# Performance work log

Measured on AMD Instinct MI355X. Metric: run time of the kernel, lower is better.

Reference implementation:

```python
import jax, jax.numpy as jnp
import numpy as np

HEADS = 24
HEAD_DIM = 96
SPARSE_N = 4
ROPE_BASE = 10000.0


def _rope_cos_sin(pos, D):
    # pos: [L] int positions; D: per-axis rotary dim (even)
    inv_freq = 1.0 / (ROPE_BASE ** (jnp.arange(0, D, 2, dtype=jnp.float32) / D))
    f = pos.astype(jnp.float32)[:, None] * inv_freq[None, :]   # [L, D/2] (interp scale = 1)
    f = jnp.concatenate([f, f], axis=-1)                        # [L, D]
    return jnp.cos(f), jnp.sin(f)


def _rotate_half(x):
    x1, x2 = jnp.split(x, 2, axis=-1)
    return jnp.concatenate([-x2, x1], axis=-1)


def _apply_rope3d(tok, frame, height, width):
    # tok: [b, h, s, d]; RoPE3D splits head_dim into 3 equal chunks for (t, y, x)
    D = tok.shape[-1] // 3
    t = jnp.repeat(jnp.arange(frame), height * width)
    y = jnp.tile(jnp.repeat(jnp.arange(height), width), frame)
    x = jnp.tile(jnp.arange(width), frame * height)
    outs = []
    for i, pos in enumerate((t, y, x)):
        cos, sin = _rope_cos_sin(pos, D)                        # [s, D]
        part = tok[..., i * D:(i + 1) * D]
        outs.append(part * cos[None, None] + _rotate_half(part) * sin[None, None])
    return jnp.concatenate(outs, axis=-1)


def _sparse_1d(x, n):
    # 'b h (g k) d -> (k b) h g d' with pad so s % n*n == 0
    b, h, s, d = x.shape
    pad = (-s) % (n * n)
    if pad:
        x = jnp.pad(x, ((0, 0), (0, 0), (0, pad), (0, 0)))
    g = (s + pad) // n
    x = x.reshape(b, h, g, n, d)
    return jnp.transpose(x, (3, 0, 1, 2, 4)).reshape(n * b, h, g, d), pad


def _reverse_sparse_1d(x, n, s):
    # '(k b) h g d -> b h (g k) d' then crop to s tokens
    kb, h, g, d = x.shape
    b = kb // n
    x = x.reshape(n, b, h, g, d)
    x = jnp.transpose(x, (1, 2, 3, 0, 4)).reshape(b, h, g * n, d)
    return x[:, :, :s, :]


def setup_inputs() -> dict:
    key = jax.random.key(0)
    ks = jax.random.split(key, 5)
    dim = HEADS * HEAD_DIM
    b, f, hh, ww = 1, 8, 16, 32
    s = f * hh * ww
    inp = {
        "hidden_states": jax.random.normal(ks[0], (b, s, dim), dtype=jnp.float32),
        "wq": jax.random.normal(ks[1], (dim, dim), dtype=jnp.float32) * 0.02,
        "bq": jnp.zeros((dim,), jnp.float32),
        "wk": jax.random.normal(ks[2], (dim, dim), dtype=jnp.float32) * 0.02,
        "bk": jnp.zeros((dim,), jnp.float32),
        "wv": jax.random.normal(ks[3], (dim, dim), dtype=jnp.float32) * 0.02,
        "bv": jnp.zeros((dim,), jnp.float32),
        "wo": jax.random.normal(ks[4], (dim, dim), dtype=jnp.float32) * 0.02,
        "bo": jnp.zeros((dim,), jnp.float32),
        "frame": f, "height": hh, "width": ww,
    }
    return inp


def reference(hidden_states, wq, bq, wk, bk, wv, bv, wo, bo, frame, height, width):
    b, s, dim = hidden_states.shape
    assert s == frame * height * width

    def proj(w, bias):
        y = hidden_states @ w + bias                            # [b, s, dim]
        return jnp.transpose(y.reshape(b, s, HEADS, HEAD_DIM), (0, 2, 1, 3))  # [b, h, s, d]

    q = proj(wq, bq)
    k = proj(wk, bk)
    v = proj(wv, bv)

    # 3D rotary embedding on q, k (self-attention path)
    q = _apply_rope3d(q, frame, height, width)
    k = _apply_rope3d(k, frame, height, width)

    # sparse-1d grouping (sparse_group=False): strided token groups of size s/sparse_n
    q, _ = _sparse_1d(q, SPARSE_N)
    k, _ = _sparse_1d(k, SPARSE_N)
    v, _ = _sparse_1d(v, SPARSE_N)

    scale = 1.0 / jnp.sqrt(jnp.asarray(HEAD_DIM, jnp.float32))
    scores = jnp.einsum('bhqd,bhkd->bhqk', q, k) * scale        # [(n b), h, g, g]
    probs = jax.nn.softmax(scores, axis=-1)
    out = jnp.einsum('bhqk,bhkd->bhqd', probs, v)

    out = _reverse_sparse_1d(out, SPARSE_N, s)                   # [b, h, s, d]
    out = jnp.transpose(out, (0, 2, 1, 3)).reshape(b, s, dim)
    return out @ wo + bo
```

## Files before the change

kernel.cpp:

```cpp
#include <hip/hip_runtime.h>
#include <stdint.h>

#define S_TOK 4096
#define DIM   2304
#define NH    24
#define DH    96
#define GQ    1024
#define KDIM  2304

typedef unsigned short ushort_t;
typedef __attribute__((ext_vector_type(8))) short bf16x8;
typedef __attribute__((ext_vector_type(4))) float f32x4;

__device__ __forceinline__ ushort_t f2bf(float x) {
    union { float f; uint32_t u; } c; c.f = x;
    uint32_t u = c.u + 0x7FFFu + ((c.u >> 16) & 1u);
    return (ushort_t)(u >> 16);
}

#define GLDS(gp, lp) __builtin_amdgcn_global_load_lds( \
    (const __attribute__((address_space(1))) void*)(gp), \
    (__attribute__((address_space(3))) void*)(lp), 16, 0, 0)

__global__ __launch_bounds__(256) void cast_bf16_kernel(const float* __restrict__ in,
                                                        ushort_t* __restrict__ out, int n4) {
    int i = blockIdx.x * 256 + threadIdx.x;
    if (i >= n4) return;
    float4 v = ((const float4*)in)[i];
    ushort4 o;
    o.x = f2bf(v.x); o.y = f2bf(v.y); o.z = f2bf(v.z); o.w = f2bf(v.w);
    ((ushort4*)out)[i] = o;
}

__global__ __launch_bounds__(256) void wtrans_kernel(const float* __restrict__ W0,
                                                     const float* __restrict__ W1,
                                                     const float* __restrict__ W2,
                                                     const float* __restrict__ W3,
                                                     ushort_t* __restrict__ WT0, int dim) {
    __shared__ float tile[32][33];
    const int z = blockIdx.z;
    const float* W = (z == 0) ? W0 : (z == 1) ? W1 : (z == 2) ? W2 : W3;
    ushort_t* WT = WT0 + (size_t)z * dim * dim;
    const int bx = blockIdx.x * 32;
    const int by = blockIdx.y * 32;
    const int tx = threadIdx.x & 31, ty = threadIdx.x >> 5;
#pragma unroll
    for (int i = 0; i < 4; ++i)
        tile[ty + i*8][tx] = W[(size_t)(by + ty + i*8) * dim + bx + tx];
    __syncthreads();
#pragma unroll
    for (int i = 0; i < 4; ++i)
        WT[(size_t)(bx + ty + i*8) * dim + by + tx] = f2bf(tile[tx][ty + i*8]);
}

template<bool FINAL>
__global__ __launch_bounds__(512, 2) void gemm256(const ushort_t* __restrict__ A,
                                                  const ushort_t* __restrict__ Bt,
                                                  const float* __restrict__ bq,
                                                  const float* __restrict__ bk,
                                                  const float* __restrict__ bv,
                                                  ushort_t* __restrict__ Qb,
                                                  ushort_t* __restrict__ Kb,
                                                  ushort_t* __restrict__ Vtb,
                                                  float* __restrict__ Cf) {
    constexpr int K  = KDIM;
    constexpr int NT = K / 32;
    __shared__ ushort_t a_s[4 * 8192];
    __shared__ ushort_t b_s[4 * 8192];
    const int t = threadIdx.x, l = t & 63, w = t >> 6;
    const int wr = w >> 2, wc = w & 3, g = l >> 4, ln = l & 15;
    const int nwg = gridDim.x * gridDim.y;
    const int lin = blockIdx.y * gridDim.x + blockIdx.x;
    const int cpx = nwg >> 3;
    const int swz = (lin & 7) * cpx + (lin >> 3);
    const int bx = swz % gridDim.x, by = swz / gridDim.x;
    const int m0 = by * 256, n0 = bx * 256;

    const int swz_rd = (g ^ ((ln >> 1) & 3)) * 8;
    const int kc_src = (((t & 3) ^ ((t >> 3) & 3)) * 8);
    const int srow   = t >> 2;

    auto stageA = [&](int kt) {
        const int slot = kt & 3;
#pragma unroll
        for (int q = 0; q < 2; ++q)
            GLDS(A + (size_t)(m0 + q*128 + srow) * K + kt*32 + kc_src,
                 &a_s[slot*8192 + (q*512 + t) * 8]);
    };
    auto stageB = [&](int kt) {
        const int slot = kt & 3;
#pragma unroll
        for (int q = 0; q < 2; ++q)
            GLDS(Bt + (size_t)(n0 + q*128 + srow) * K + kt*32 + kc_src,
                 &b_s[slot*8192 + (q*512 + t) * 8]);
    };

    f32x4 acc[8][4] = {};

    stageA(0); stageB(0); stageA(1); stageB(1); stageA(2); stageB(2);
    asm volatile("s_waitcnt vmcnt(8)" ::: "memory");
    __builtin_amdgcn_s_barrier();

    for (int kt = 0; kt < NT; ++kt) {
        const int slot = kt & 3;
        bf16x8 bv4[4];
        {
            bf16x8 av[4];
#pragma unroll
            for (int j = 0; j < 4; ++j)
                bv4[j] = *(const bf16x8*)&b_s[slot*8192 + (wc*64 + j*16 + ln)*32 + swz_rd];
#pragma unroll
            for (int i = 0; i < 4; ++i)
                av[i] = *(const bf16x8*)&a_s[slot*8192 + (wr*128 + i*16 + ln)*32 + swz_rd];
            if (kt < NT - 3) stageA(kt + 3);
            __builtin_amdgcn_s_barrier();
            asm volatile("s_waitcnt lgkmcnt(0)" ::: "memory");
            __builtin_amdgcn_sched_barrier(0);
            __builtin_amdgcn_s_setprio(1);
#pragma unroll
            for (int i = 0; i < 4; ++i)
#pragma unroll
                for (int j = 0; j < 4; ++j)
                    acc[i][j] = __builtin_amdgcn_mfma_f32_16x16x32_bf16(av[i], bv4[j], acc[i][j], 0, 0, 0);
            __builtin_amdgcn_s_setprio(0);
        }
        {
            bf16x8 av[4];
#pragma unroll
            for (int i = 0; i < 4; ++i)
                av[i] = *(const bf16x8*)&a_s[slot*8192 + (wr*128 + 64 + i*16 + ln)*32 + swz_rd];
            if (kt < NT - 3) stageB(kt + 3);
            if (kt <= NT - 4)      asm volatile("s_waitcnt vmcnt(8)" ::: "memory");
            else if (kt == NT - 3) asm volatile("s_waitcnt vmcnt(4)" ::: "memory");
            else                   asm volatile("s_waitcnt vmcnt(0)" ::: "memory");
            __builtin_amdgcn_s_barrier();
            asm volatile("s_waitcnt lgkmcnt(0)" ::: "memory");
            __builtin_amdgcn_sched_barrier(0);
            __builtin_amdgcn_s_setprio(1);
#pragma unroll
            for (int i = 0; i < 4; ++i)
#pragma unroll
                for (int j = 0; j < 4; ++j)
                    acc[4 + i][j] = __builtin_amdgcn_mfma_f32_16x16x32_bf16(av[i], bv4[j], acc[4 + i][j], 0, 0, 0);
            __builtin_amdgcn_s_setprio(0);
        }
    }

    if constexpr (FINAL) {
        const float* bias = bq;
#pragma unroll
        for (int i = 0; i < 8; ++i) {
            int mb = m0 + wr*128 + i*16 + g*4;
#pragma unroll
            for (int j = 0; j < 4; ++j) {
                int n = n0 + wc*64 + j*16 + ln;
                float bb = bias[n];
#pragma unroll
                for (int r = 0; r < 4; ++r)
                    Cf[(size_t)(mb + r) * DIM + n] = acc[i][j][r] + bb;
            }
        }
    } else {
        const int mode = bx / 9;
        const int nb = (bx - mode * 9) * 256;
        const float* bias = (mode == 0) ? bq : (mode == 1) ? bk : bv;
        if (mode == 2) {
#pragma unroll
            for (int i = 0; i < 8; ++i) {
                int mb = m0 + wr*128 + i*16 + g*4;
                int q  = mb >> 2;
#pragma unroll
                for (int j = 0; j < 4; ++j) {
                    int nm = nb + wc*64 + j*16 + ln;
                    int hh = nm / DH, d = nm - hh * DH;
                    float bb = bias[nm];
#pragma unroll
                    for (int r = 0; r < 4; ++r)
                        Vtb[(size_t)(r * NH + hh) * (DH * GQ) + (size_t)d * GQ + q] =
                            f2bf(acc[i][j][r] + bb);
                }
            }
        } else {
            ushort_t* O = (mode == 0) ? Qb : Kb;
            const float scq = (mode == 0) ? 0.1020620726159658f : 1.0f;
#pragma unroll
            for (int i = 0; i < 8; ++i) {
                int mb = m0 + wr*128 + i*16 + g*4;
#pragma unroll
                for (int jp = 0; jp < 2; ++jp) {
                    int j  = jp * 2;
                    int n1 = nb + wc*64 + j*16 + ln;
                    int hh = n1 / DH, d1 = n1 - hh * DH;
                    int sec = d1 >> 5, f = d1 & 15;
                    float invf = __expf((float)f * -0.5756462732485114f);
                    float b1 = bias[n1], b2 = bias[n1 + 16];
#pragma unroll
                    for (int r = 0; r < 4; ++r) {
                        int m = mb + r;
                        int pos = (sec == 0) ? (m >> 9) : (sec == 1) ? ((m >> 5) & 15) : (m & 31);
                        float ang = (float)pos * invf;
                        float sn, cs;
                        __sincosf(ang, &sn, &cs);
                        float v1 = acc[i][j][r]     + b1;
                        float v2 = acc[i][j + 1][r] + b2;
                        size_t base = ((size_t)((m & 3) * NH + hh)) * (GQ * DH) + (size_t)(m >> 2) * DH;
                        O[base + d1]      = f2bf((v1 * cs - v2 * sn) * scq);
                        O[base + d1 + 16] = f2bf((v2 * cs + v1 * sn) * scq);
                    }
                }
            }
        }
    }
}

__global__ __launch_bounds__(128, 2) void attn_kernel(const ushort_t* __restrict__ Qb,
                                                      const ushort_t* __restrict__ Kb,
                                                      const ushort_t* __restrict__ Vt,
                                                      ushort_t* __restrict__ ATT) {
    __shared__ ushort_t k_s[2][12 * 64 * 8];
    __shared__ ushort_t v_s[8 * 96 * 8];
    __shared__ ushort_t p_s[2 * 4 * 16 * 64];

    const int t = threadIdx.x, l = t & 63, w = t >> 6, g = l >> 4, ln = l & 15;
    const int lin  = blockIdx.x;
    const int swz  = (lin & 7) * 96 + (lin >> 3);
    const int inst = swz >> 3;
    const int qb0  = (swz & 7) * 128;
    const int n_idx = inst / NH, h = inst - n_idx * NH;
    const int swzp = (ln & 7) << 3;

    const ushort_t* Qi = Qb + (size_t)inst * (GQ * DH);
    const ushort_t* Ki = Kb + (size_t)inst * (GQ * DH);
    const ushort_t* Vi = Vt + (size_t)inst * (DH * GQ);

    auto stageK = [&](int kt, int b) {
#pragma unroll
        for (int it = 0; it < 6; ++it) {
            int P = t + it * 128;
            int c = P >> 6, key = P & 63;
            GLDS(Ki + (size_t)(kt * 64 + key) * DH + c * 8, &k_s[b][P * 8]);
        }
    };
    auto stageV = [&](int kt) {
#pragma unroll
        for (int it = 0; it < 6; ++it) {
            int P = t + it * 128;
            int c = P / 96, d = P - c * 96;
            GLDS(Vi + (size_t)d * GQ + kt * 64 + c * 8, &v_s[P * 8]);
        }
    };

    bf16x8 qf[4][3];
#pragma unroll
    for (int qt = 0; qt < 4; ++qt)
#pragma unroll
        for (int ks = 0; ks < 3; ++ks)
            qf[qt][ks] = *(const bf16x8*)(Qi + (size_t)(qb0 + w*64 + qt*16 + ln) * DH + ks*32 + g*8);

    float m_run[4], l_run[4];
#pragma unroll
    for (int qt = 0; qt < 4; ++qt) { m_run[qt] = -3.0e38f; l_run[qt] = 0.f; }
    f32x4 acc_o[4][6] = {};

    stageK(0, 0);
    stageV(0);
    __syncthreads();

    int cur = 0;
    for (int kt = 0; kt < 16; ++kt) {
        stageK((kt + 1) & 15, cur ^ 1);
        float al4[4];

#pragma unroll
        for (int qp = 0; qp < 2; ++qp) {
            f32x4 sc[2][4] = {};
#pragma unroll
            for (int ct = 0; ct < 4; ++ct) {
                bf16x8 kf0 = *(const bf16x8*)&k_s[cur][((0*4 + g)*64 + ct*16 + ln) * 8];
                bf16x8 kf1 = *(const bf16x8*)&k_s[cur][((1*4 + g)*64 + ct*16 + ln) * 8];
                bf16x8 kf2 = *(const bf16x8*)&k_s[cur][((2*4 + g)*64 + ct*16 + ln) * 8];
#pragma unroll
                for (int qi = 0; qi < 2; ++qi) {
                    sc[qi][ct] = __builtin_amdgcn_mfma_f32_16x16x32_bf16(kf0, qf[qp*2+qi][0], sc[qi][ct], 0, 0, 0);
                    sc[qi][ct] = __builtin_amdgcn_mfma_f32_16x16x32_bf16(kf1, qf[qp*2+qi][1], sc[qi][ct], 0, 0, 0);
                    sc[qi][ct] = __builtin_amdgcn_mfma_f32_16x16x32_bf16(kf2, qf[qp*2+qi][2], sc[qi][ct], 0, 0, 0);
                }
            }
#pragma unroll
            for (int qi = 0; qi < 2; ++qi) {
                const int qt = qp*2 + qi;
                float mx = sc[qi][0][0];
#pragma unroll
                for (int ct = 0; ct < 4; ++ct)
#pragma unroll
                    for (int r = 0; r < 4; ++r)
                        mx = fmaxf(mx, sc[qi][ct][r]);
                mx = fmaxf(mx, __shfl_xor(mx, 16, 64));
                mx = fmaxf(mx, __shfl_xor(mx, 32, 64));
                float mn = fmaxf(m_run[qt], mx);
                float al = __expf(m_run[qt] - mn);
                m_run[qt] = mn;
                float rs = 0.f;
                ushort_t pb[16];
#pragma unroll
                for (int ct = 0; ct < 4; ++ct)
#pragma unroll
                    for (int r = 0; r < 4; ++r) {
                        float p = __expf(sc[qi][ct][r] - mn);
                        rs += p;
                        pb[ct*4 + r] = f2bf(p);
                    }
                rs += __shfl_xor(rs, 16, 64);
                rs += __shfl_xor(rs, 32, 64);
                l_run[qt] = l_run[qt] * al + rs;
                al4[qt] = al;
                const int pbase = ((w*4 + qt)*16 + ln) * 64;
#pragma unroll
                for (int ct = 0; ct < 4; ++ct) {
                    ushort4 pk;
                    pk.x = pb[ct*4+0]; pk.y = pb[ct*4+1]; pk.z = pb[ct*4+2]; pk.w = pb[ct*4+3];
                    *(ushort4*)&p_s[pbase + ((ct*16 + g*4) ^ swzp)] = pk;
                }
            }
        }

#pragma unroll
        for (int qt = 0; qt < 4; ++qt)
#pragma unroll
            for (int r = 0; r < 4; ++r) {
                float a = __shfl(al4[qt], g*4 + r, 16);
#pragma unroll
                for (int dt = 0; dt < 6; ++dt)
                    acc_o[qt][dt][r] *= a;
            }

        asm volatile("s_waitcnt vmcnt(6)" ::: "memory");
        __builtin_amdgcn_s_barrier();
        __builtin_amdgcn_sched_barrier(0);
        asm volatile("s_waitcnt lgkmcnt(0)" ::: "memory");
        __builtin_amdgcn_sched_barrier(0);

#pragma unroll
        for (int kb = 0; kb < 2; ++kb) {
            bf16x8 pf4[4];
#pragma unroll
            for (int qt = 0; qt < 4; ++qt)
                pf4[qt] = *(const bf16x8*)&p_s[((w*4 + qt)*16 + ln)*64 + ((kb*32 + g*8) ^ swzp)];
#pragma unroll
            for (int dt = 0; dt < 6; ++dt) {
                bf16x8 vf = *(const bf16x8*)&v_s[((kb*4 + g)*96 + dt*16 + ln) * 8];
#pragma unroll
                for (int qt = 0; qt < 4; ++qt)
                    acc_o[qt][dt] = __builtin_amdgcn_mfma_f32_16x16x32_bf16(pf4[qt], vf, acc_o[qt][dt], 0, 0, 0);
            }
        }

        __syncthreads();
        if (kt < 15) stageV(kt + 1);
        cur ^= 1;
    }

#pragma unroll
    for (int qt = 0; qt < 4; ++qt) {
        float inv = 1.0f / l_run[qt];
#pragma unroll
        for (int r = 0; r < 4; ++r) {
            float iv = __shfl(inv, g*4 + r, 16);
            int gq = qb0 + w*64 + qt*16 + g*4 + r;
            size_t base = ((size_t)(gq * 4 + n_idx)) * DIM + h * DH;
#pragma unroll
            for (int dt = 0; dt < 6; ++dt)
                ATT[base + dt*16 + ln] = f2bf(acc_o[qt][dt][r] * iv);
        }
    }
}

extern "C" void kernel_launch(void* const* d_in, const int* in_sizes, int n_in,
                              void* d_out, int out_size, void* d_ws, size_t ws_size,
                              hipStream_t stream) {
    const float* hidden = (const float*)d_in[0];
    const float* wq = (const float*)d_in[1];
    const float* bq = (const float*)d_in[2];
    const float* wk = (const float*)d_in[3];
    const float* bk = (const float*)d_in[4];
    const float* wv = (const float*)d_in[5];
    const float* bv = (const float*)d_in[6];
    const float* wo = (const float*)d_in[7];
    const float* bo = (const float*)d_in[8];
    float* out = (float*)d_out;

    char* ws = (char*)d_ws;
    ushort_t* Xb  = (ushort_t*)ws;
    ushort_t* WTq = (ushort_t*)(ws + 18874368);
    ushort_t* WTk = WTq + (size_t)DIM * DIM;
    ushort_t* WTv = WTk + (size_t)DIM * DIM;
    ushort_t* WTo = WTv + (size_t)DIM * DIM;
    ushort_t* Qb  = WTo + (size_t)DIM * DIM;
    ushort_t* Kb  = Qb + (size_t)S_TOK * DIM;
    ushort_t* Vtb = Kb + (size_t)S_TOK * DIM;
    ushort_t* ATT = Vtb + (size_t)S_TOK * DIM;

    cast_bf16_kernel<<<dim3(9216), dim3(256), 0, stream>>>(hidden, Xb, (S_TOK * DIM) / 4);

    wtrans_kernel<<<dim3(72, 72, 4), 256, 0, stream>>>(wq, wk, wv, wo, WTq, DIM);

    gemm256<false><<<dim3(27, 16), 512, 0, stream>>>(Xb, WTq, bq, bk, bv, Qb, Kb, Vtb, nullptr);

    attn_kernel<<<dim3(768), 128, 0, stream>>>(Qb, Kb, Vtb, ATT);

    gemm256<true><<<dim3(9, 16), 512, 0, stream>>>(ATT, WTo, bo, nullptr, nullptr,
                                                   nullptr, nullptr, nullptr, out);
}
```

Before: 354.6 us.

## Restructure GEMM main loop to K=64 half-tiles with 5-slot LDS ring

Reworks the bf16 GEMM pipeline so each LDS stage holds a 128-row half tile with 64 K-elements, using an 8-way XOR swizzle and a 5-deep ring buffer in place of 4 slots of K=32. Each loop iteration now processes 64 of K in four MFMA phases, with loads issued between phases and extra barriers around each compute block. The aim is to halve loop overhead per K element and keep more global loads in flight. In exchange it uses more LDS per workgroup, which may affect the 2-blocks-per-CU occupancy target, and adds barriers whose cost may offset the gains.

```diff
diff --git a/kernel.cpp b/kernel.cpp
--- a/kernel.cpp
+++ b/kernel.cpp
@@ -63,10 +63,11 @@
                                                   ushort_t* __restrict__ Kb,
                                                   ushort_t* __restrict__ Vtb,
                                                   float* __restrict__ Cf) {
-    constexpr int K  = KDIM;
-    constexpr int NT = K / 32;
-    __shared__ ushort_t a_s[4 * 8192];
-    __shared__ ushort_t b_s[4 * 8192];
+    constexpr int K   = KDIM;
+    constexpr int NT  = K / 64;
+    constexpr int NH2 = 2 * NT;
+    __shared__ ushort_t a_s[5 * 8192];
+    __shared__ ushort_t b_s[5 * 8192];
     const int t = threadIdx.x, l = t & 63, w = t >> 6;
     const int wr = w >> 2, wc = w & 3, g = l >> 4, ln = l & 15;
     const int nwg = gridDim.x * gridDim.y;
@@ -76,74 +77,110 @@
     const int bx = swz % gridDim.x, by = swz / gridDim.x;
     const int m0 = by * 256, n0 = bx * 256;
 
-    const int swz_rd = (g ^ ((ln >> 1) & 3)) * 8;
-    const int kc_src = (((t & 3) ^ ((t >> 3) & 3)) * 8);
-    const int srow   = t >> 2;
-
-    auto stageA = [&](int kt) {
-        const int slot = kt & 3;
-#pragma unroll
-        for (int q = 0; q < 2; ++q)
-            GLDS(A + (size_t)(m0 + q*128 + srow) * K + kt*32 + kc_src,
-                 &a_s[slot*8192 + (q*512 + t) * 8]);
+    const int c_src8 = (((t & 7) ^ ((t >> 3) & 7)) * 8);
+    const int srow   = t >> 3;
+
+    auto stageA = [&](int h) {
+        if (h >= NH2) return;
+        const ushort_t* base = A + (size_t)(m0 + (h & 1) * 128 + srow) * K
+                                 + (size_t)(h >> 1) * 64 + c_src8;
+        ushort_t* dst = a_s + (h % 5) * 8192 + t * 8;
+        GLDS(base, dst);
+        GLDS(base + (size_t)64 * K, dst + 4096);
     };
-    auto stageB = [&](int kt) {
-        const int slot = kt & 3;
-#pragma unroll
-        for (int q = 0; q < 2; ++q)
-            GLDS(Bt + (size_t)(n0 + q*128 + srow) * K + kt*32 + kc_src,
-                 &b_s[slot*8192 + (q*512 + t) * 8]);
+    auto stageB = [&](int h) {
+        if (h >= NH2) return;
+        const ushort_t* base = Bt + (size_t)(n0 + (h & 1) * 128 + srow) * K
+                                  + (size_t)(h >> 1) * 64 + c_src8;
+        ushort_t* dst = b_s + (h % 5) * 8192 + t * 8;
+        GLDS(base, dst);
+        GLDS(base + (size_t)64 * K, dst + 4096);
     };
 
+    const int rd_c0 = (g ^ (ln & 7)) * 8;
+    const int rd_c1 = rd_c0 ^ 32;
+
     f32x4 acc[8][4] = {};
 
     stageA(0); stageB(0); stageA(1); stageB(1); stageA(2); stageB(2);
-    asm volatile("s_waitcnt vmcnt(8)" ::: "memory");
+    asm volatile("s_waitcnt vmcnt(4)" ::: "memory");
     __builtin_amdgcn_s_barrier();
 
-    for (int kt = 0; kt < NT; ++kt) {
-        const int slot = kt & 3;
-        bf16x8 bv4[4];
-        {
-            bf16x8 av[4];
+    for (int tk = 0; tk < NT; ++tk) {
+        const ushort_t* a_base = a_s + ((2*tk + wr) % 5) * 8192 + ln * 64;
+        const ushort_t* b_base = b_s + ((2*tk + (wc >> 1)) % 5) * 8192
+                                     + ((wc & 1) * 64 + ln) * 64;
+        bf16x8 bv4[4], av[4];
+
+        stageA(2*tk + 3);
+#pragma unroll
+        for (int j = 0; j < 4; ++j) bv4[j] = *(const bf16x8*)&b_base[j*1024 + rd_c0];
+#pragma unroll
+        for (int i = 0; i < 4; ++i) av[i]  = *(const bf16x8*)&a_base[i*1024 + rd_c0];
+        __builtin_amdgcn_s_barrier();
+        asm volatile("s_waitcnt lgkmcnt(0)" ::: "memory");
+        __builtin_amdgcn_sched_barrier(0);
+        __builtin_amdgcn_s_setprio(1);
+#pragma unroll
+        for (int i = 0; i < 4; ++i)
 #pragma unroll
             for (int j = 0; j < 4; ++j)
-                bv4[j] = *(const bf16x8*)&b_s[slot*8192 + (wc*64 + j*16 + ln)*32 + swz_rd];
-#pragma unroll
-            for (int i = 0; i < 4; ++i)
-                av[i] = *(const bf16x8*)&a_s[slot*8192 + (wr*128 + i*16 + ln)*32 + swz_rd];
-            if (kt < NT - 3) stageA(kt + 3);
-            __builtin_amdgcn_s_barrier();
-            asm volatile("s_waitcnt lgkmcnt(0)" ::: "memory");
-            __builtin_amdgcn_sched_barrier(0);
-            __builtin_amdgcn_s_setprio(1);
-#pragma unroll
-            for (int i = 0; i < 4; ++i)
-#pragma unroll
-                for (int j = 0; j < 4; ++j)
-                    acc[i][j] = __builtin_amdgcn_mfma_f32_16x16x32_bf16(av[i], bv4[j], acc[i][j], 0, 0, 0);
-            __builtin_amdgcn_s_setprio(0);
-        }
-        {
-            bf16x8 av[4];
-#pragma unroll
-            for (int i = 0; i < 4; ++i)
-                av[i] = *(const bf16x8*)&a_s[slot*8192 + (wr*128 + 64 + i*16 + ln)*32 + swz_rd];
-            if (kt < NT - 3) stageB(kt + 3);
-            if (kt <= NT - 4)      asm volatile("s_waitcnt vmcnt(8)" ::: "memory");
-            else if (kt == NT - 3) asm volatile("s_waitcnt vmcnt(4)" ::: "memory");
-            else                   asm volatile("s_waitcnt vmcnt(0)" ::: "memory");
-            __builtin_amdgcn_s_barrier();
-            asm volatile("s_waitcnt lgkmcnt(0)" ::: "memory");
-            __builtin_amdgcn_sched_barrier(0);
-            __builtin_amdgcn_s_setprio(1);
-#pragma unroll
-            for (int i = 0; i < 4; ++i)
-#pragma unroll
-                for (int j = 0; j < 4; ++j)
-                    acc[4 + i][j] = __builtin_amdgcn_mfma_f32_16x16x32_bf16(av[i], bv4[j], acc[4 + i][j], 0, 0, 0);
-            __builtin_amdgcn_s_setprio(0);
-        }
+                acc[i][j] = __builtin_amdgcn_mfma_f32_16x16x32_bf16(av[i], bv4[j], acc[i][j], 0, 0, 0);
+        __builtin_amdgcn_s_setprio(0);
+        __builtin_amdgcn_sched_barrier(0);
+        __builtin_amdgcn_s_barrier();
+
+        stageB(2*tk + 3);
+#pragma unroll
+        for (int i = 0; i < 4; ++i) av[i] = *(const bf16x8*)&a_base[(4+i)*1024 + rd_c0];
+        __builtin_amdgcn_s_barrier();
+        asm volatile("s_waitcnt lgkmcnt(0)" ::: "memory");
+        __builtin_amdgcn_sched_barrier(0);
+        __builtin_amdgcn_s_setprio(1);
+#pragma unroll
+        for (int i = 0; i < 4; ++i)
+#pragma unroll
+            for (int j = 0; j < 4; ++j)
+                acc[4+i][j] = __builtin_amdgcn_mfma_f32_16x16x32_bf16(av[i], bv4[j], acc[4+i][j], 0, 0, 0);
+        __builtin_amdgcn_s_setprio(0);
+        __builtin_amdgcn_sched_barrier(0);
+        __builtin_amdgcn_s_barrier();
+
+        stageA(2*tk + 4);
+#pragma unroll
+        for (int j = 0; j < 4; ++j) bv4[j] = *(const bf16x8*)&b_base[j*1024 + rd_c1];
+#pragma unroll
+        for (int i = 0; i < 4; ++i) av[i]  = *(const bf16x8*)&a_base[i*1024 + rd_c1];
+        __builtin_amdgcn_s_barrier();
+        asm volatile("s_waitcnt lgkmcnt(0)" ::: "memory");
+        __builtin_amdgcn_sched_barrier(0);
+        __builtin_amdgcn_s_setprio(1);
+#pragma unroll
+        for (int i = 0; i < 4; ++i)
+#pragma unroll
+            for (int j = 0; j < 4; ++j)
+                acc[i][j] = __builtin_amdgcn_mfma_f32_16x16x32_bf16(av[i], bv4[j], acc[i][j], 0, 0, 0);
+        __builtin_amdgcn_s_setprio(0);
+        __builtin_amdgcn_sched_barrier(0);
+        __builtin_amdgcn_s_barrier();
+
+        stageB(2*tk + 4);
+#pragma unroll
+        for (int i = 0; i < 4; ++i) av[i] = *(const bf16x8*)&a_base[(4+i)*1024 + rd_c1];
+        if (tk < NT - 2)       asm volatile("s_waitcnt vmcnt(4)" ::: "memory");
+        else if (tk == NT - 2) asm volatile("s_waitcnt vmcnt(0)" ::: "memory");
+        __builtin_amdgcn_s_barrier();
+        asm volatile("s_waitcnt lgkmcnt(0)" ::: "memory");
+        __builtin_amdgcn_sched_barrier(0);
+        __builtin_amdgcn_s_setprio(1);
+#pragma unroll
+        for (int i = 0; i < 4; ++i)
+#pragma unroll
+            for (int j = 0; j < 4; ++j)
+                acc[4+i][j] = __builtin_amdgcn_mfma_f32_16x16x32_bf16(av[i], bv4[j], acc[4+i][j], 0, 0, 0);
+        __builtin_amdgcn_s_setprio(0);
+        __builtin_amdgcn_sched_barrier(0);
+        __builtin_amdgcn_s_barrier();
     }
 
     if constexpr (FINAL) {
```

Result: slower. 409.3 us (+15.4%).
